# Kernel optimization log

Hardware: AMD Instinct MI355X
Metric: run time of the kernel (lower is better)

The kernel has to match this reference:

```python
import jax, jax.numpy as jnp
import numpy as np


def setup_inputs() -> dict:
    key = jax.random.key(0)
    qkv = jax.random.normal(key, (2, 1536, 4096), dtype=jnp.float32)
    return {"qkv": qkv, "num_heads": 8}


def reference(qkv, num_heads):
    bs, width, length = qkv.shape
    ch = width // (3 * num_heads)
    # [B*H, 3*ch, T] -> split into q, k, v each [B*H, ch, T]
    qkv_h = qkv.reshape(bs * num_heads, 3 * ch, length)
    q, k, v = qkv_h[:, :ch], qkv_h[:, ch:2 * ch], qkv_h[:, 2 * ch:]
    scale = 1.0 / np.sqrt(np.sqrt(ch)).astype(np.float32)
    # scores: [B*H, T, T]
    weight = jnp.einsum('bct,bcs->bts', q * scale, k * scale)
    weight = jax.nn.softmax(weight.astype(jnp.float32), axis=-1).astype(weight.dtype)
    a = jnp.einsum('bts,bcs->bct', weight, v)  # [B*H, ch, T]
    return a.reshape(bs, num_heads * ch, length)
```

## Files before the change

### kernel.cpp

```cpp
#include <hip/hip_runtime.h>
#include <hip/hip_bf16.h>

typedef __bf16 bf16x8 __attribute__((ext_vector_type(8)));
typedef __bf16 bf16x4 __attribute__((ext_vector_type(4)));
typedef __bf16 bf16x2 __attribute__((ext_vector_type(2)));
typedef float  f32x4  __attribute__((ext_vector_type(4)));

#define T_LEN 4096
#define QBLK  128
#define NT    64

__device__ __forceinline__ int swz(int row, int colByte) {
    return row * 128 + (colByte ^ (((row ^ (row >> 2)) & 7) << 4));
}
__device__ __forceinline__ int swzM(int row, int colByte) {
    return row * 128 + (colByte ^ ((row & 7) << 4));
}
__device__ __forceinline__ int swzO(int row, int colByte) {
    return row * 512 + (colByte ^ ((row & 7) << 5));
}

#define QSCALE 0.18033688011112042f

#if __has_builtin(__builtin_amdgcn_exp2f)
#define EXP2(x) __builtin_amdgcn_exp2f(x)
#else
__device__ __forceinline__ float EXP2(float x) {
    float r; asm("v_exp_f32 %0, %1" : "=v"(r) : "v"(x)); return r;
}
#endif

__device__ __forceinline__ void glds16(const void* g, void* l) {
    __builtin_amdgcn_global_load_lds(
        (const __attribute__((address_space(1))) void*)g,
        (__attribute__((address_space(3))) void*)l, 16, 0, 0);
}

__global__ __launch_bounds__(256)
void qkv_prepass(const float* __restrict__ qkv, char* __restrict__ kpan,
                 char* __restrict__ vpan) {
    const int tile = blockIdx.x;
    const int bh   = blockIdx.y;
    const float* kp = qkv + ((size_t)bh * 192 + 64)  * T_LEN + tile * 64;
    const float* vp = qkv + ((size_t)bh * 192 + 128) * T_LEN + tile * 64;
    char* kout = kpan + (size_t)(bh * 64 + tile) * 8192;
    char* vout = vpan + (size_t)(bh * 64 + tile) * 8192;

    const int t  = threadIdx.x;
    const int s  = t & 63;
    const int o4 = t >> 6;
    #pragma unroll
    for (int oo = 0; oo < 2; ++oo) {
        const int oct = o4 + oo * 4;
        bf16x8 v;
        #pragma unroll
        for (int j = 0; j < 8; ++j)
            v[j] = (__bf16)kp[(size_t)(oct * 8 + j) * T_LEN + s];
        *(bf16x8*)(kout + swz(s, oct * 16)) = v;
    }
    const int c = t & 63;
    #pragma unroll
    for (int p = 0; p < 4; ++p) {
        const int u = o4 * 4 + p;
        float4 f = *(const float4*)(vp + (size_t)c * T_LEN + u * 4);
        const int up = (u & 8) | ((u & 3) << 1) | ((u >> 2) & 1);
        bf16x4 hv;
        hv[0] = (__bf16)f.x; hv[1] = (__bf16)f.y;
        hv[2] = (__bf16)f.z; hv[3] = (__bf16)f.w;
        *(bf16x4*)(vout + swz(c, up * 8)) = hv;
    }
}

__global__ __launch_bounds__(512, 4)
void qkv_attn_glds(const float* __restrict__ qkv, float* __restrict__ out,
                   const char* __restrict__ kpan, const char* __restrict__ vpan) {
    __shared__ __align__(16) char lds[81920];

    const int fid   = (blockIdx.x & 7) * 64 + (blockIdx.x >> 3);
    const int bh    = fid >> 5;
    const int ttile = fid & 31;
    const float* qp = qkv + (size_t)bh * 192 * T_LEN;
    const char* kpb = kpan + (size_t)bh * 64 * 8192;
    const char* vpb = vpan + (size_t)bh * 64 * 8192;
    const int t0 = ttile * QBLK;

    const int tid  = threadIdx.x;
    const int wave = tid >> 6, lane = tid & 63;
    const int g = lane >> 4, i = lane & 15;
    const int tg = wave >> 1, half = wave & 1;

    glds16(kpb + tid * 16,        lds + 16384 + wave * 1024);
    glds16(vpb + tid * 16,        lds + 49152 + wave * 1024);
    glds16(kpb + 8192 + tid * 16, lds + 16384 + 8192 + wave * 1024);
    glds16(vpb + 8192 + tid * 16, lds + 49152 + 8192 + wave * 1024);

    {
        const int tq  = (tid & 31) * 4;
        const int cp8 = tid >> 5;
        #pragma unroll
        for (int hh = 0; hh < 2; ++hh) {
            const int cpair = cp8 + hh * 16;
            const float* base = qp + (size_t)(cpair * 2) * T_LEN + t0 + tq;
            float4 lo = *(const float4*)(base);
            float4 hi = *(const float4*)(base + T_LEN);
            bf16x2 v;
            v[0] = (__bf16)(lo.x * QSCALE); v[1] = (__bf16)(hi.x * QSCALE);
            *(bf16x2*)(lds + swz(tq + 0, cpair * 4)) = v;
            v[0] = (__bf16)(lo.y * QSCALE); v[1] = (__bf16)(hi.y * QSCALE);
            *(bf16x2*)(lds + swz(tq + 1, cpair * 4)) = v;
            v[0] = (__bf16)(lo.z * QSCALE); v[1] = (__bf16)(hi.z * QSCALE);
            *(bf16x2*)(lds + swz(tq + 2, cpair * 4)) = v;
            v[0] = (__bf16)(lo.w * QSCALE); v[1] = (__bf16)(hi.w * QSCALE);
            *(bf16x2*)(lds + swz(tq + 3, cpair * 4)) = v;
        }
    }
    __syncthreads();
    bf16x8 qreg[2][2];
    #pragma unroll
    for (int h = 0; h < 2; ++h)
        #pragma unroll
        for (int kk = 0; kk < 2; ++kk)
            qreg[h][kk] = *(const bf16x8*)(lds + swz(tg * 32 + h * 16 + i, kk * 64 + g * 16));

    f32x4 oacc[2][4];
    #pragma unroll
    for (int h = 0; h < 2; ++h)
        #pragma unroll
        for (int n = 0; n < 4; ++n) oacc[h][n] = (f32x4){0.f, 0.f, 0.f, 0.f};
    float l0 = 0.f, l1 = 0.f;

    for (int t = 0; t < NT; ++t) {
        if (t + 2 < NT) {
            const size_t off = (size_t)(t + 2) * 8192;
            const int b = (t + 2) & 3;
            glds16(kpb + off + tid * 16, lds + 16384 + b * 8192 + wave * 1024);
            glds16(vpb + off + tid * 16, lds + 49152 + b * 8192 + wave * 1024);
            asm volatile("s_waitcnt vmcnt(4)\n\ts_barrier" ::: "memory");
        } else if (t + 2 == NT) {
            asm volatile("s_waitcnt vmcnt(2)\n\ts_barrier" ::: "memory");
        } else {
            asm volatile("s_waitcnt vmcnt(0)\n\ts_barrier" ::: "memory");
        }
        char* KsR = lds + 16384 + (t & 3) * 8192;
        char* VsR = lds + 49152 + (t & 3) * 8192;

        f32x4 sacc[2][2];
        #pragma unroll
        for (int h = 0; h < 2; ++h)
            #pragma unroll
            for (int mt = 0; mt < 2; ++mt) sacc[h][mt] = (f32x4){0.f, 0.f, 0.f, 0.f};
        __builtin_amdgcn_s_setprio(1);
        #pragma unroll
        for (int kk = 0; kk < 2; ++kk)
            #pragma unroll
            for (int mt = 0; mt < 2; ++mt) {
                bf16x8 kf = *(const bf16x8*)(KsR + swz(half * 32 + mt * 16 + i, kk * 64 + g * 16));
                sacc[0][mt] = __builtin_amdgcn_mfma_f32_16x16x32_bf16(kf, qreg[0][kk], sacc[0][mt], 0, 0, 0);
                sacc[1][mt] = __builtin_amdgcn_mfma_f32_16x16x32_bf16(kf, qreg[1][kk], sacc[1][mt], 0, 0, 0);
            }
        __builtin_amdgcn_s_setprio(0);

        bf16x8 pa0, pa1;
        #pragma unroll
        for (int r = 0; r < 4; ++r) {
            float a0 = EXP2(sacc[0][0][r]);
            float a1 = EXP2(sacc[0][1][r]);
            l0 += a0 + a1;
            pa0[r] = (__bf16)a0; pa0[4 + r] = (__bf16)a1;
            float b0 = EXP2(sacc[1][0][r]);
            float b1 = EXP2(sacc[1][1][r]);
            l1 += b0 + b1;
            pa1[r] = (__bf16)b0; pa1[4 + r] = (__bf16)b1;
        }

        __builtin_amdgcn_s_setprio(1);
        #pragma unroll
        for (int n = 0; n < 4; ++n) {
            bf16x8 bv = *(const bf16x8*)(VsR + swz(n * 16 + i, half * 64 + g * 16));
            oacc[0][n] = __builtin_amdgcn_mfma_f32_16x16x32_bf16(pa0, bv, oacc[0][n], 0, 0, 0);
            oacc[1][n] = __builtin_amdgcn_mfma_f32_16x16x32_bf16(pa1, bv, oacc[1][n], 0, 0, 0);
        }
        __builtin_amdgcn_s_setprio(0);
    }
    l0 += __shfl_xor(l0, 16); l0 += __shfl_xor(l0, 32);
    l1 += __shfl_xor(l1, 16); l1 += __shfl_xor(l1, 32);

    __syncthreads();
    char* mbase = lds + 16384 + tg * 8192;
    float* lbase = (float*)(lds);
    if (half == 1) {
        #pragma unroll
        for (int h = 0; h < 2; ++h)
            #pragma unroll
            for (int n = 0; n < 4; ++n)
                *(f32x4*)(mbase + swzM(n * 16 + i, h * 64 + g * 16)) = oacc[h][n];
        if (g == 0) { lbase[tg * 32 + i] = l0; lbase[tg * 32 + 16 + i] = l1; }
    }
    __syncthreads();
    if (half == 0) {
        #pragma unroll
        for (int h = 0; h < 2; ++h)
            #pragma unroll
            for (int n = 0; n < 4; ++n)
                oacc[h][n] += *(const f32x4*)(mbase + swzM(n * 16 + i, h * 64 + g * 16));
        l0 += lbase[tg * 32 + i];
        l1 += lbase[tg * 32 + 16 + i];
    }
    __syncthreads();
    if (half == 0) {
        #pragma unroll
        for (int h = 0; h < 2; ++h) {
            float invl = 1.0f / (h ? l1 : l0);
            #pragma unroll
            for (int reg = 0; reg < 4; ++reg) {
                float inv_r = __shfl(invl, g * 4 + reg);
                int t_loc = tg * 32 + h * 16 + g * 4 + reg;
                #pragma unroll
                for (int n = 0; n < 4; ++n) {
                    int c = n * 16 + i;
                    *(float*)(lds + swzO(c, t_loc * 4)) = oacc[h][n][reg] * inv_r;
                }
            }
        }
    }
    __syncthreads();
    #pragma unroll
    for (int it = 0; it < 4; ++it) {
        int idx = it * 512 + tid;
        int c   = idx >> 5;
        int seg = idx & 31;
        float4 u = *(const float4*)(lds + swzO(c, seg * 16));
        *(float4*)(out + (size_t)(bh * 64 + c) * T_LEN + t0 + seg * 4) = u;
    }
}

__global__ __launch_bounds__(256)
void simple_attn(const float* __restrict__ qkv, float* __restrict__ out) {
    const int wave = threadIdx.x >> 6;
    const int lane = threadIdx.x & 63;
    const int t  = blockIdx.x * 4 + wave;
    const int bh = blockIdx.y;
    const float* qp = qkv + (size_t)bh * 192 * T_LEN;
    const float* kp = qp + (size_t)64  * T_LEN;
    const float* vp = qp + (size_t)128 * T_LEN;
    const float qc = qp[(size_t)lane * T_LEN + t] * 0.125f;
    float m = -1e30f, l = 0.f, o = 0.f;
    for (int s = 0; s < T_LEN; ++s) {
        float prod = qc * kp[(size_t)lane * T_LEN + s];
        #pragma unroll
        for (int d = 1; d < 64; d <<= 1) prod += __shfl_xor(prod, d);
        const float nm   = fmaxf(m, prod);
        const float corr = __expf(m - nm);
        const float p    = __expf(prod - nm);
        l = l * corr + p;
        o = o * corr + p * vp[(size_t)lane * T_LEN + s];
        m = nm;
    }
    out[(size_t)(bh * 64 + lane) * T_LEN + t] = o / l;
}

extern "C" void kernel_launch(void* const* d_in, const int* in_sizes, int n_in,
                              void* d_out, int out_size, void* d_ws, size_t ws_size,
                              hipStream_t stream) {
    const float* qkv = (const float*)d_in[0];
    float* out = (float*)d_out;
    const size_t pan_bytes = (size_t)16 * 64 * 8192;
    if (ws_size >= 2 * pan_bytes) {
        char* kpan = (char*)d_ws;
        char* vpan = kpan + pan_bytes;
        qkv_prepass<<<dim3(64, 16), 256, 0, stream>>>(qkv, kpan, vpan);
        qkv_attn_glds<<<dim3(512), 512, 0, stream>>>(qkv, out, kpan, vpan);
    } else {
        simple_attn<<<dim3(T_LEN / 4, 16), 256, 0, stream>>>(qkv, out);
    }
}
```

Before: 90.53 us.

## Load K/V fragments directly from L2 into registers, dropping LDS staging

The prepass now writes K and V panels in MFMA fragment order, so each lane can read its operand with one 16-byte global load per fragment. The attention kernel drops the LDS ring buffer, the global_load_lds prefetch and the per-tile barrier. Instead it holds K/V fragments in registers and prefetches the next tile right after each MFMA phase. This aims to remove barrier and LDS traffic from the inner loop and to cut LDS size. In exchange the loop depends on L2 latency being hidden by only a one-step register prefetch, and it uses more registers.

```diff
diff --git a/kernel.cpp b/kernel.cpp
--- a/kernel.cpp
+++ b/kernel.cpp
@@ -2,8 +2,6 @@
 #include <hip/hip_bf16.h>
 
 typedef __bf16 bf16x8 __attribute__((ext_vector_type(8)));
-typedef __bf16 bf16x4 __attribute__((ext_vector_type(4)));
-typedef __bf16 bf16x2 __attribute__((ext_vector_type(2)));
 typedef float  f32x4  __attribute__((ext_vector_type(4)));
 
 #define T_LEN 4096
@@ -29,12 +27,6 @@
     float r; asm("v_exp_f32 %0, %1" : "=v"(r) : "v"(x)); return r;
 }
 #endif
-
-__device__ __forceinline__ void glds16(const void* g, void* l) {
-    __builtin_amdgcn_global_load_lds(
-        (const __attribute__((address_space(1))) void*)g,
-        (__attribute__((address_space(3))) void*)l, 16, 0, 0);
-}
 
 __global__ __launch_bounds__(256)
 void qkv_prepass(const float* __restrict__ qkv, char* __restrict__ kpan,
@@ -46,42 +38,51 @@
     char* kout = kpan + (size_t)(bh * 64 + tile) * 8192;
     char* vout = vpan + (size_t)(bh * 64 + tile) * 8192;
 
-    const int t  = threadIdx.x;
-    const int s  = t & 63;
-    const int o4 = t >> 6;
-    #pragma unroll
-    for (int oo = 0; oo < 2; ++oo) {
-        const int oct = o4 + oo * 4;
-        bf16x8 v;
-        #pragma unroll
-        for (int j = 0; j < 8; ++j)
-            v[j] = (__bf16)kp[(size_t)(oct * 8 + j) * T_LEN + s];
-        *(bf16x8*)(kout + swz(s, oct * 16)) = v;
-    }
-    const int c = t & 63;
-    #pragma unroll
-    for (int p = 0; p < 4; ++p) {
-        const int u = o4 * 4 + p;
-        float4 f = *(const float4*)(vp + (size_t)c * T_LEN + u * 4);
-        const int up = (u & 8) | ((u & 3) << 1) | ((u >> 2) & 1);
-        bf16x4 hv;
-        hv[0] = (__bf16)f.x; hv[1] = (__bf16)f.y;
-        hv[2] = (__bf16)f.z; hv[3] = (__bf16)f.w;
-        *(bf16x4*)(vout + swz(c, up * 8)) = hv;
+    const int t = threadIdx.x;
+    {
+        const int s = t & 63;
+        const int o4 = t >> 6;
+        #pragma unroll
+        for (int oo = 0; oo < 2; ++oo) {
+            const int oct = o4 + oo * 4;
+            bf16x8 v;
+            #pragma unroll
+            for (int j = 0; j < 8; ++j)
+                v[j] = (__bf16)kp[(size_t)(oct * 8 + j) * T_LEN + s];
+            const int chunk   = ((s >> 5) * 2 + (oct >> 2)) * 2 + ((s >> 4) & 1);
+            const int lanepos = (oct & 3) * 16 + (s & 15);
+            *(bf16x8*)(kout + chunk * 1024 + lanepos * 16) = v;
+        }
+    }
+    {
+        const int c = t & 63;
+        #pragma unroll
+        for (int lp = 0; lp < 2; ++lp) {
+            const int hg = (t >> 6) + lp * 4;
+            const int hf = hg >> 2, gg = hg & 3;
+            float4 f0 = *(const float4*)(vp + (size_t)c * T_LEN + hf * 32 + gg * 4);
+            float4 f1 = *(const float4*)(vp + (size_t)c * T_LEN + hf * 32 + 16 + gg * 4);
+            bf16x8 v;
+            v[0] = (__bf16)f0.x; v[1] = (__bf16)f0.y;
+            v[2] = (__bf16)f0.z; v[3] = (__bf16)f0.w;
+            v[4] = (__bf16)f1.x; v[5] = (__bf16)f1.y;
+            v[6] = (__bf16)f1.z; v[7] = (__bf16)f1.w;
+            const int chunk   = hf * 4 + (c >> 4);
+            const int lanepos = gg * 16 + (c & 15);
+            *(bf16x8*)(vout + chunk * 1024 + lanepos * 16) = v;
+        }
     }
 }
 
 __global__ __launch_bounds__(512, 4)
-void qkv_attn_glds(const float* __restrict__ qkv, float* __restrict__ out,
-                   const char* __restrict__ kpan, const char* __restrict__ vpan) {
-    __shared__ __align__(16) char lds[81920];
+void qkv_attn_l2(const float* __restrict__ qkv, float* __restrict__ out,
+                 const char* __restrict__ kpan, const char* __restrict__ vpan) {
+    __shared__ __align__(16) char lds[49152];
 
     const int fid   = (blockIdx.x & 7) * 64 + (blockIdx.x >> 3);
     const int bh    = fid >> 5;
     const int ttile = fid & 31;
     const float* qp = qkv + (size_t)bh * 192 * T_LEN;
-    const char* kpb = kpan + (size_t)bh * 64 * 8192;
-    const char* vpb = vpan + (size_t)bh * 64 * 8192;
     const int t0 = ttile * QBLK;
 
     const int tid  = threadIdx.x;
@@ -89,10 +90,8 @@
     const int g = lane >> 4, i = lane & 15;
     const int tg = wave >> 1, half = wave & 1;
 
-    glds16(kpb + tid * 16,        lds + 16384 + wave * 1024);
-    glds16(vpb + tid * 16,        lds + 49152 + wave * 1024);
-    glds16(kpb + 8192 + tid * 16, lds + 16384 + 8192 + wave * 1024);
-    glds16(vpb + 8192 + tid * 16, lds + 49152 + 8192 + wave * 1024);
+    const char* kbase = kpan + (size_t)bh * 64 * 8192 + half * 4096 + lane * 16;
+    const char* vbase = vpan + (size_t)bh * 64 * 8192 + half * 4096 + lane * 16;
 
     {
         const int tq  = (tid & 31) * 4;
@@ -103,16 +102,26 @@
             const float* base = qp + (size_t)(cpair * 2) * T_LEN + t0 + tq;
             float4 lo = *(const float4*)(base);
             float4 hi = *(const float4*)(base + T_LEN);
-            bf16x2 v;
-            v[0] = (__bf16)(lo.x * QSCALE); v[1] = (__bf16)(hi.x * QSCALE);
-            *(bf16x2*)(lds + swz(tq + 0, cpair * 4)) = v;
-            v[0] = (__bf16)(lo.y * QSCALE); v[1] = (__bf16)(hi.y * QSCALE);
-            *(bf16x2*)(lds + swz(tq + 1, cpair * 4)) = v;
-            v[0] = (__bf16)(lo.z * QSCALE); v[1] = (__bf16)(hi.z * QSCALE);
-            *(bf16x2*)(lds + swz(tq + 2, cpair * 4)) = v;
-            v[0] = (__bf16)(lo.w * QSCALE); v[1] = (__bf16)(hi.w * QSCALE);
-            *(bf16x2*)(lds + swz(tq + 3, cpair * 4)) = v;
-        }
+            __bf16 v0, v1;
+            v0 = (__bf16)(lo.x * QSCALE); v1 = (__bf16)(hi.x * QSCALE);
+            *(__bf16*)(lds + swz(tq + 0, cpair * 4)) = v0;
+            *(__bf16*)(lds + swz(tq + 0, cpair * 4) + 2) = v1;
+            v0 = (__bf16)(lo.y * QSCALE); v1 = (__bf16)(hi.y * QSCALE);
+            *(__bf16*)(lds + swz(tq + 1, cpair * 4)) = v0;
+            *(__bf16*)(lds + swz(tq + 1, cpair * 4) + 2) = v1;
+            v0 = (__bf16)(lo.z * QSCALE); v1 = (__bf16)(hi.z * QSCALE);
+            *(__bf16*)(lds + swz(tq + 2, cpair * 4)) = v0;
+            *(__bf16*)(lds + swz(tq + 2, cpair * 4) + 2) = v1;
+            v0 = (__bf16)(lo.w * QSCALE); v1 = (__bf16)(hi.w * QSCALE);
+            *(__bf16*)(lds + swz(tq + 3, cpair * 4)) = v0;
+            *(__bf16*)(lds + swz(tq + 3, cpair * 4) + 2) = v1;
+        }
+    }
+    bf16x8 kf[4], vf[4];
+    #pragma unroll
+    for (int q = 0; q < 4; ++q) {
+        kf[q] = *(const bf16x8*)(kbase + q * 1024);
+        vf[q] = *(const bf16x8*)(vbase + q * 1024);
     }
     __syncthreads();
     bf16x8 qreg[2][2];
@@ -130,20 +139,6 @@
     float l0 = 0.f, l1 = 0.f;
 
     for (int t = 0; t < NT; ++t) {
-        if (t + 2 < NT) {
-            const size_t off = (size_t)(t + 2) * 8192;
-            const int b = (t + 2) & 3;
-            glds16(kpb + off + tid * 16, lds + 16384 + b * 8192 + wave * 1024);
-            glds16(vpb + off + tid * 16, lds + 49152 + b * 8192 + wave * 1024);
-            asm volatile("s_waitcnt vmcnt(4)\n\ts_barrier" ::: "memory");
-        } else if (t + 2 == NT) {
-            asm volatile("s_waitcnt vmcnt(2)\n\ts_barrier" ::: "memory");
-        } else {
-            asm volatile("s_waitcnt vmcnt(0)\n\ts_barrier" ::: "memory");
-        }
-        char* KsR = lds + 16384 + (t & 3) * 8192;
-        char* VsR = lds + 49152 + (t & 3) * 8192;
-
         f32x4 sacc[2][2];
         #pragma unroll
         for (int h = 0; h < 2; ++h)
@@ -154,11 +149,15 @@
         for (int kk = 0; kk < 2; ++kk)
             #pragma unroll
             for (int mt = 0; mt < 2; ++mt) {
-                bf16x8 kf = *(const bf16x8*)(KsR + swz(half * 32 + mt * 16 + i, kk * 64 + g * 16));
-                sacc[0][mt] = __builtin_amdgcn_mfma_f32_16x16x32_bf16(kf, qreg[0][kk], sacc[0][mt], 0, 0, 0);
-                sacc[1][mt] = __builtin_amdgcn_mfma_f32_16x16x32_bf16(kf, qreg[1][kk], sacc[1][mt], 0, 0, 0);
+                sacc[0][mt] = __builtin_amdgcn_mfma_f32_16x16x32_bf16(kf[kk * 2 + mt], qreg[0][kk], sacc[0][mt], 0, 0, 0);
+                sacc[1][mt] = __builtin_amdgcn_mfma_f32_16x16x32_bf16(kf[kk * 2 + mt], qreg[1][kk], sacc[1][mt], 0, 0, 0);
             }
         __builtin_amdgcn_s_setprio(0);
+        if (t + 1 < NT) {
+            const char* kn = kbase + (size_t)(t + 1) * 8192;
+            #pragma unroll
+            for (int q = 0; q < 4; ++q) kf[q] = *(const bf16x8*)(kn + q * 1024);
+        }
 
         bf16x8 pa0, pa1;
         #pragma unroll
@@ -176,11 +175,15 @@
         __builtin_amdgcn_s_setprio(1);
         #pragma unroll
         for (int n = 0; n < 4; ++n) {
-            bf16x8 bv = *(const bf16x8*)(VsR + swz(n * 16 + i, half * 64 + g * 16));
-            oacc[0][n] = __builtin_amdgcn_mfma_f32_16x16x32_bf16(pa0, bv, oacc[0][n], 0, 0, 0);
-            oacc[1][n] = __builtin_amdgcn_mfma_f32_16x16x32_bf16(pa1, bv, oacc[1][n], 0, 0, 0);
+            oacc[0][n] = __builtin_amdgcn_mfma_f32_16x16x32_bf16(pa0, vf[n], oacc[0][n], 0, 0, 0);
+            oacc[1][n] = __builtin_amdgcn_mfma_f32_16x16x32_bf16(pa1, vf[n], oacc[1][n], 0, 0, 0);
         }
         __builtin_amdgcn_s_setprio(0);
+        if (t + 1 < NT) {
+            const char* vn = vbase + (size_t)(t + 1) * 8192;
+            #pragma unroll
+            for (int q = 0; q < 4; ++q) vf[q] = *(const bf16x8*)(vn + q * 1024);
+        }
     }
     l0 += __shfl_xor(l0, 16); l0 += __shfl_xor(l0, 32);
     l1 += __shfl_xor(l1, 16); l1 += __shfl_xor(l1, 32);
@@ -269,7 +272,7 @@
         char* kpan = (char*)d_ws;
         char* vpan = kpan + pan_bytes;
         qkv_prepass<<<dim3(64, 16), 256, 0, stream>>>(qkv, kpan, vpan);
-        qkv_attn_glds<<<dim3(512), 512, 0, stream>>>(qkv, out, kpan, vpan);
+        qkv_attn_l2<<<dim3(512), 512, 0, stream>>>(qkv, out, kpan, vpan);
     } else {
         simple_attn<<<dim3(T_LEN / 4, 16), 256, 0, stream>>>(qkv, out);
     }
```

New measurement: 95.36 us. 1.05x slower.
